# Optimization experiments

Measured on AMD Instinct MI355X. Metric: run time of the kernel, lower is better.

The kernel has to match this reference:

```python
import jax, jax.numpy as jnp
import numpy as np

HIDDEN_DIM = 1000
CONTEXT_DIM = 2000


def setup_inputs() -> dict:
    key = jax.random.key(0)
    k1, k2, k3, k4 = jax.random.split(key, 4)
    B, N = 64, 1024
    std = 0.001
    return {
        "s_prev": jax.random.normal(k1, (B, HIDDEN_DIM), dtype=jnp.float32),
        "h_j": jax.random.normal(k2, (B, N, CONTEXT_DIM), dtype=jnp.float32),
        "W_a": jax.random.normal(k3, (HIDDEN_DIM, HIDDEN_DIM), dtype=jnp.float32) * std,
        "U_a": jax.random.normal(k4, (HIDDEN_DIM, CONTEXT_DIM), dtype=jnp.float32) * std,
        "v_a": jnp.zeros((HIDDEN_DIM,), dtype=jnp.float32),
    }


def reference(s_prev, h_j, W_a, U_a, v_a):
    # W_a s: (B, H); U_a h: (B, N, H)
    W_a_s = jnp.einsum("bd,hd->bh", s_prev, W_a)
    U_a_h = jnp.einsum("bnc,hc->bnh", h_j, U_a)
    energy = jnp.tanh(W_a_s[:, None, :] + U_a_h)  # (B, N, H)
    scores = jnp.einsum("bnh,h->bn", energy, v_a)  # (B, N)
    return scores
```

## Files before the change

kernel.cpp:

```cpp
#include <hip/hip_runtime.h>
#include <hip/hip_bf16.h>

#define HID 1000
#define CTX 2000
#define KP   2016
#define HP   1024
#define BATCH 64
#define NSEQ 1024
#define M_TOT (BATCH * NSEQ)
#define WSTR 1024

typedef __attribute__((ext_vector_type(8))) short short8;
typedef __attribute__((ext_vector_type(4))) float floatx4;

__device__ __forceinline__ unsigned short f2bf(float x) {
    union { float f; unsigned u; } v; v.f = x;
    unsigned r = v.u + 0x7FFFu + ((v.u >> 16) & 1u);
    return (unsigned short)(r >> 16);
}

typedef const __attribute__((address_space(1))) unsigned glb_u32;
typedef __attribute__((address_space(3))) unsigned lds_u32;
__device__ __forceinline__ void gload16(const void* g, void* l) {
    __builtin_amdgcn_global_load_lds((glb_u32*)g, (lds_u32*)l, 16, 0, 0);
}

__global__ void zero_kernel(float* __restrict__ out, int n) {
    int i = blockIdx.x * 256 + threadIdx.x;
    if (i < n) out[i] = 0.0f;
}

__global__ void convertA_kernel(const float* __restrict__ src, unsigned short* __restrict__ dst) {
    int row = blockIdx.x;
    int t = threadIdx.x;
    if (t >= KP / 8) return;
    unsigned short pk[8];
    if (t < CTX / 8) {
        const float* p = src + (size_t)row * CTX + t * 8;
        float4 a = *(const float4*)p;
        float4 b = *(const float4*)(p + 4);
        pk[0]=f2bf(a.x); pk[1]=f2bf(a.y); pk[2]=f2bf(a.z); pk[3]=f2bf(a.w);
        pk[4]=f2bf(b.x); pk[5]=f2bf(b.y); pk[6]=f2bf(b.z); pk[7]=f2bf(b.w);
    } else {
#pragma unroll
        for (int i = 0; i < 8; i++) pk[i] = 0;
    }
    *(short8*)(dst + (size_t)row * KP + t * 8) = *(short8*)pk;
}

__global__ void convertB_kernel(const float* __restrict__ src, unsigned short* __restrict__ dst) {
    int row = blockIdx.x;
    int t = threadIdx.x;
    if (t >= KP / 8) return;
    unsigned short pk[8];
    if (row < HID && t < CTX / 8) {
        const float* p = src + (size_t)row * CTX + t * 8;
        float4 a = *(const float4*)p;
        float4 b = *(const float4*)(p + 4);
        pk[0]=f2bf(a.x); pk[1]=f2bf(a.y); pk[2]=f2bf(a.z); pk[3]=f2bf(a.w);
        pk[4]=f2bf(b.x); pk[5]=f2bf(b.y); pk[6]=f2bf(b.z); pk[7]=f2bf(b.w);
    } else {
#pragma unroll
        for (int i = 0; i < 8; i++) pk[i] = 0;
    }
    *(short8*)(dst + (size_t)row * KP + t * 8) = *(short8*)pk;
}

__global__ void ws_kernel(const float* __restrict__ s_prev,
                          const float* __restrict__ W_a,
                          float* __restrict__ W_s) {
    int wave = threadIdx.x >> 6, lane = threadIdx.x & 63;
    int gw = blockIdx.x * 4 + wave;
    int b = gw / HID, h = gw % HID;
    const float* wr = W_a + (size_t)h * HID;
    const float* sr = s_prev + (size_t)b * HID;
    float acc = 0.0f;
#pragma unroll
    for (int it = 0; it < 4; ++it) {
        int idx = it * 64 + lane;
        if (idx < HID / 4) {
            float4 w = *(const float4*)(wr + idx * 4);
            float4 s = *(const float4*)(sr + idx * 4);
            acc += w.x * s.x + w.y * s.y + w.z * s.z + w.w * s.w;
        }
    }
    acc += __shfl_xor(acc, 1);
    acc += __shfl_xor(acc, 2);
    acc += __shfl_xor(acc, 4);
    acc += __shfl_xor(acc, 8);
    acc += __shfl_xor(acc, 16);
    acc += __shfl_xor(acc, 32);
    if (lane == 0) W_s[b * WSTR + h] = acc;
}

__global__ __launch_bounds__(256) void gemm_kernel(
        const unsigned short* __restrict__ A, const unsigned short* __restrict__ B,
        const float* __restrict__ W_s, const float* __restrict__ v_a,
        float* __restrict__ out) {
    __shared__ __align__(16) unsigned short As[128 * 32];
    __shared__ __align__(16) unsigned short Bs[128 * 32];

    const int tid  = threadIdx.x;
    const int lane = tid & 63;
    const int wave = tid >> 6;
    const int wm = wave & 1, wh = wave >> 1;
    const int ln = lane & 15, quad = lane >> 4;

    const int h0 = blockIdx.x * 128;
    const int m0 = blockIdx.y * 128;
    const int b  = m0 >> 10;

    const int srow = lane >> 2;
    const int scol = (lane & 3) * 8;
    const unsigned short* aptr0 = A + (size_t)(m0 + wave * 16 + srow) * KP + scol;
    const unsigned short* aptr1 = aptr0 + (size_t)64 * KP;
    const unsigned short* bptr0 = B + (size_t)(h0 + wave * 16 + srow) * KP + scol;
    const unsigned short* bptr1 = bptr0 + (size_t)64 * KP;
    unsigned short* asl0 = &As[(wave * 16) * 32];
    unsigned short* asl1 = &As[(64 + wave * 16) * 32];
    unsigned short* bsl0 = &Bs[(wave * 16) * 32];
    unsigned short* bsl1 = &Bs[(64 + wave * 16) * 32];

    floatx4 acc[4][4];
#pragma unroll
    for (int i = 0; i < 4; i++)
#pragma unroll
        for (int j = 0; j < 4; j++) acc[i][j] = (floatx4)0.0f;

    for (int kk = 0; kk < KP / 32; ++kk) {
        __syncthreads();
        gload16(aptr0, asl0);
        gload16(aptr1, asl1);
        gload16(bptr0, bsl0);
        gload16(bptr1, bsl1);
        aptr0 += 32; aptr1 += 32; bptr0 += 32; bptr1 += 32;
        __syncthreads();

        short8 af[4], bfr[4];
#pragma unroll
        for (int i = 0; i < 4; i++)
            af[i] = *(const short8*)&As[(wm * 64 + i * 16 + ln) * 32 + quad * 8];
#pragma unroll
        for (int j = 0; j < 4; j++)
            bfr[j] = *(const short8*)&Bs[(wh * 64 + j * 16 + ln) * 32 + quad * 8];
#pragma unroll
        for (int i = 0; i < 4; i++)
#pragma unroll
            for (int j = 0; j < 4; j++)
                acc[i][j] = __builtin_amdgcn_mfma_f32_16x16x32_bf16(af[i], bfr[j], acc[i][j], 0, 0, 0);
    }

    float rowsum[4][4];
#pragma unroll
    for (int i = 0; i < 4; i++)
#pragma unroll
        for (int r = 0; r < 4; r++) rowsum[i][r] = 0.0f;

#pragma unroll
    for (int j = 0; j < 4; j++) {
        const int h = h0 + wh * 64 + j * 16 + ln;
        float wsv = 0.0f, vav = 0.0f;
        if (h < HID) { wsv = W_s[b * WSTR + h]; vav = v_a[h]; }
#pragma unroll
        for (int i = 0; i < 4; i++)
#pragma unroll
            for (int r = 0; r < 4; r++)
                rowsum[i][r] += vav * tanhf(acc[i][j][r] + wsv);
    }

#pragma unroll
    for (int i = 0; i < 4; i++)
#pragma unroll
        for (int r = 0; r < 4; r++) {
            float v = rowsum[i][r];
            v += __shfl_xor(v, 1);
            v += __shfl_xor(v, 2);
            v += __shfl_xor(v, 4);
            v += __shfl_xor(v, 8);
            rowsum[i][r] = v;
        }

    if (ln == 0) {
#pragma unroll
        for (int i = 0; i < 4; i++) {
            const int row = m0 + wm * 64 + i * 16 + quad * 4;
#pragma unroll
            for (int r = 0; r < 4; r++)
                atomicAdd(&out[row + r], rowsum[i][r]);
        }
    }
}

__global__ __launch_bounds__(256) void attn_fallback(
        const float* __restrict__ h_j, const float* __restrict__ U_a,
        const float* __restrict__ W_s, const float* __restrict__ v_a,
        float* __restrict__ out) {
    __shared__ unsigned short As[128 * 40];
    __shared__ unsigned short Bs[128 * 40];
    const int tid = threadIdx.x, lane = tid & 63, wave = tid >> 6;
    const int wm = wave & 1, wh = wave >> 1, ln = lane & 15, quad = lane >> 4;
    const int h0 = blockIdx.x * 128, m0 = blockIdx.y * 128, b = m0 >> 10;
    const int srow = tid >> 1, scol = (tid & 1) * 16;
    const float* aptr = h_j + (size_t)(m0 + srow) * CTX;
    const int gh = h0 + srow;
    const bool bvalid = (gh < HID);
    const float* bptr = U_a + (size_t)(bvalid ? gh : 0) * CTX;
    floatx4 acc[4][4];
#pragma unroll
    for (int i = 0; i < 4; i++)
#pragma unroll
        for (int j = 0; j < 4; j++) acc[i][j] = (floatx4)0.0f;
    for (int kk = 0; kk < 63; ++kk) {
        const int c = kk * 32 + scol;
        short8 apk0 = (short8)0, apk1 = (short8)0, bpk0 = (short8)0, bpk1 = (short8)0;
        if (c < CTX) {
            float4 t0 = *(const float4*)(aptr + c), t1 = *(const float4*)(aptr + c + 4);
            float4 t2 = *(const float4*)(aptr + c + 8), t3 = *(const float4*)(aptr + c + 12);
            apk0[0]=(short)f2bf(t0.x); apk0[1]=(short)f2bf(t0.y); apk0[2]=(short)f2bf(t0.z); apk0[3]=(short)f2bf(t0.w);
            apk0[4]=(short)f2bf(t1.x); apk0[5]=(short)f2bf(t1.y); apk0[6]=(short)f2bf(t1.z); apk0[7]=(short)f2bf(t1.w);
            apk1[0]=(short)f2bf(t2.x); apk1[1]=(short)f2bf(t2.y); apk1[2]=(short)f2bf(t2.z); apk1[3]=(short)f2bf(t2.w);
            apk1[4]=(short)f2bf(t3.x); apk1[5]=(short)f2bf(t3.y); apk1[6]=(short)f2bf(t3.z); apk1[7]=(short)f2bf(t3.w);
        }
        if (bvalid && c < CTX) {
            float4 t0 = *(const float4*)(bptr + c), t1 = *(const float4*)(bptr + c + 4);
            float4 t2 = *(const float4*)(bptr + c + 8), t3 = *(const float4*)(bptr + c + 12);
            bpk0[0]=(short)f2bf(t0.x); bpk0[1]=(short)f2bf(t0.y); bpk0[2]=(short)f2bf(t0.z); bpk0[3]=(short)f2bf(t0.w);
            bpk0[4]=(short)f2bf(t1.x); bpk0[5]=(short)f2bf(t1.y); bpk0[6]=(short)f2bf(t1.z); bpk0[7]=(short)f2bf(t1.w);
            bpk1[0]=(short)f2bf(t2.x); bpk1[1]=(short)f2bf(t2.y); bpk1[2]=(short)f2bf(t2.z); bpk1[3]=(short)f2bf(t2.w);
            bpk1[4]=(short)f2bf(t3.x); bpk1[5]=(short)f2bf(t3.y); bpk1[6]=(short)f2bf(t3.z); bpk1[7]=(short)f2bf(t3.w);
        }
        __syncthreads();
        *(short8*)&As[srow * 40 + scol]     = apk0;
        *(short8*)&As[srow * 40 + scol + 8] = apk1;
        *(short8*)&Bs[srow * 40 + scol]     = bpk0;
        *(short8*)&Bs[srow * 40 + scol + 8] = bpk1;
        __syncthreads();
        short8 af[4], bfr[4];
#pragma unroll
        for (int i = 0; i < 4; i++) af[i] = *(const short8*)&As[(wm * 64 + i * 16 + ln) * 40 + quad * 8];
#pragma unroll
        for (int j = 0; j < 4; j++) bfr[j] = *(const short8*)&Bs[(wh * 64 + j * 16 + ln) * 40 + quad * 8];
#pragma unroll
        for (int i = 0; i < 4; i++)
#pragma unroll
            for (int j = 0; j < 4; j++)
                acc[i][j] = __builtin_amdgcn_mfma_f32_16x16x32_bf16(af[i], bfr[j], acc[i][j], 0, 0, 0);
    }
    float rowsum[4][4];
#pragma unroll
    for (int i = 0; i < 4; i++)
#pragma unroll
        for (int r = 0; r < 4; r++) rowsum[i][r] = 0.0f;
#pragma unroll
    for (int j = 0; j < 4; j++) {
        const int h = h0 + wh * 64 + j * 16 + ln;
        float wsv = 0.0f, vav = 0.0f;
        if (h < HID) { wsv = W_s[b * WSTR + h]; vav = v_a[h]; }
#pragma unroll
        for (int i = 0; i < 4; i++)
#pragma unroll
            for (int r = 0; r < 4; r++)
                rowsum[i][r] += vav * tanhf(acc[i][j][r] + wsv);
    }
#pragma unroll
    for (int i = 0; i < 4; i++)
#pragma unroll
        for (int r = 0; r < 4; r++) {
            float v = rowsum[i][r];
            v += __shfl_xor(v, 1); v += __shfl_xor(v, 2);
            v += __shfl_xor(v, 4); v += __shfl_xor(v, 8);
            rowsum[i][r] = v;
        }
    if (ln == 0) {
#pragma unroll
        for (int i = 0; i < 4; i++) {
            const int row = m0 + wm * 64 + i * 16 + quad * 4;
#pragma unroll
            for (int r = 0; r < 4; r++) atomicAdd(&out[row + r], rowsum[i][r]);
        }
    }
}

extern "C" void kernel_launch(void* const* d_in, const int* in_sizes, int n_in,
                              void* d_out, int out_size, void* d_ws, size_t ws_size,
                              hipStream_t stream) {
    const float* s_prev = (const float*)d_in[0];
    const float* h_j    = (const float*)d_in[1];
    const float* W_a    = (const float*)d_in[2];
    const float* U_a    = (const float*)d_in[3];
    const float* v_a    = (const float*)d_in[4];
    float* out = (float*)d_out;

    const size_t ws_off   = 0;
    const size_t b_off    = 64 * WSTR * sizeof(float);
    const size_t a_off    = b_off + (size_t)HP * KP * sizeof(short);
    const size_t need     = a_off + (size_t)M_TOT * KP * sizeof(short);

    float* W_s = (float*)((char*)d_ws + ws_off);

    zero_kernel<<<dim3(M_TOT / 256), 256, 0, stream>>>(out, M_TOT);
    ws_kernel<<<dim3(BATCH * HID / 4), 256, 0, stream>>>(s_prev, W_a, W_s);

    if (ws_size >= need) {
        unsigned short* B_bf = (unsigned short*)((char*)d_ws + b_off);
        unsigned short* A_bf = (unsigned short*)((char*)d_ws + a_off);
        convertA_kernel<<<dim3(M_TOT), 256, 0, stream>>>(h_j, A_bf);
        convertB_kernel<<<dim3(HP), 256, 0, stream>>>(U_a, B_bf);
        gemm_kernel<<<dim3(HP / 128, M_TOT / 128), 256, 0, stream>>>(A_bf, B_bf, W_s, v_a, out);
    } else {
        attn_fallback<<<dim3(HP / 128, M_TOT / 128), 256, 0, stream>>>(h_j, U_a, W_s, v_a, out);
    }
}
```

Before: 1.222 ms.

## Loop over all hidden tiles inside each GEMM block, accumulating row sums locally

Each block now owns a 128-row M tile and iterates over all eight 128-wide hidden tiles, keeping the tanh-weighted row sums in registers instead of launching one block per (h, m) pair. This cuts the number of atomicAdds to the output and lets the A tile be re-read from L2 by the same block. It also adds a launch bound of 2 blocks per CU and removes the fallback path that ran when workspace was too small. The grid shrinks from 4096 to 512 blocks, which risks under-filling the GPU and serialises the work per block.

```diff
diff --git a/kernel.cpp b/kernel.cpp
--- a/kernel.cpp
+++ b/kernel.cpp
@@ -93,7 +93,7 @@
     if (lane == 0) W_s[b * WSTR + h] = acc;
 }
 
-__global__ __launch_bounds__(256) void gemm_kernel(
+__global__ __launch_bounds__(256, 2) void gemm_kernel(
         const unsigned short* __restrict__ A, const unsigned short* __restrict__ B,
         const float* __restrict__ W_s, const float* __restrict__ v_a,
         float* __restrict__ out) {
@@ -106,66 +106,70 @@
     const int wm = wave & 1, wh = wave >> 1;
     const int ln = lane & 15, quad = lane >> 4;
 
-    const int h0 = blockIdx.x * 128;
-    const int m0 = blockIdx.y * 128;
+    const int m0 = blockIdx.x * 128;
     const int b  = m0 >> 10;
 
     const int srow = lane >> 2;
     const int scol = (lane & 3) * 8;
-    const unsigned short* aptr0 = A + (size_t)(m0 + wave * 16 + srow) * KP + scol;
-    const unsigned short* aptr1 = aptr0 + (size_t)64 * KP;
-    const unsigned short* bptr0 = B + (size_t)(h0 + wave * 16 + srow) * KP + scol;
-    const unsigned short* bptr1 = bptr0 + (size_t)64 * KP;
+    const unsigned short* abase0 = A + (size_t)(m0 + wave * 16 + srow) * KP + scol;
+    const unsigned short* abase1 = abase0 + (size_t)64 * KP;
     unsigned short* asl0 = &As[(wave * 16) * 32];
     unsigned short* asl1 = &As[(64 + wave * 16) * 32];
     unsigned short* bsl0 = &Bs[(wave * 16) * 32];
     unsigned short* bsl1 = &Bs[(64 + wave * 16) * 32];
 
-    floatx4 acc[4][4];
+    float rowsum[4][4];
 #pragma unroll
     for (int i = 0; i < 4; i++)
 #pragma unroll
-        for (int j = 0; j < 4; j++) acc[i][j] = (floatx4)0.0f;
-
-    for (int kk = 0; kk < KP / 32; ++kk) {
-        __syncthreads();
-        gload16(aptr0, asl0);
-        gload16(aptr1, asl1);
-        gload16(bptr0, bsl0);
-        gload16(bptr1, bsl1);
-        aptr0 += 32; aptr1 += 32; bptr0 += 32; bptr1 += 32;
-        __syncthreads();
-
-        short8 af[4], bfr[4];
+        for (int r = 0; r < 4; r++) rowsum[i][r] = 0.0f;
+
+    for (int ht = 0; ht < HP / 128; ++ht) {
+        const unsigned short* aptr0 = abase0;
+        const unsigned short* aptr1 = abase1;
+        const unsigned short* bptr0 = B + (size_t)(ht * 128 + wave * 16 + srow) * KP + scol;
+        const unsigned short* bptr1 = bptr0 + (size_t)64 * KP;
+
+        floatx4 acc[4][4];
 #pragma unroll
         for (int i = 0; i < 4; i++)
-            af[i] = *(const short8*)&As[(wm * 64 + i * 16 + ln) * 32 + quad * 8];
-#pragma unroll
-        for (int j = 0; j < 4; j++)
-            bfr[j] = *(const short8*)&Bs[(wh * 64 + j * 16 + ln) * 32 + quad * 8];
-#pragma unroll
-        for (int i = 0; i < 4; i++)
+#pragma unroll
+            for (int j = 0; j < 4; j++) acc[i][j] = (floatx4)0.0f;
+
+        for (int kk = 0; kk < KP / 32; ++kk) {
+            __syncthreads();
+            gload16(aptr0, asl0);
+            gload16(aptr1, asl1);
+            gload16(bptr0, bsl0);
+            gload16(bptr1, bsl1);
+            aptr0 += 32; aptr1 += 32; bptr0 += 32; bptr1 += 32;
+            __syncthreads();
+
+            short8 af[4], bfr[4];
+#pragma unroll
+            for (int i = 0; i < 4; i++)
+                af[i] = *(const short8*)&As[(wm * 64 + i * 16 + ln) * 32 + quad * 8];
 #pragma unroll
             for (int j = 0; j < 4; j++)
-                acc[i][j] = __builtin_amdgcn_mfma_f32_16x16x32_bf16(af[i], bfr[j], acc[i][j], 0, 0, 0);
-    }
-
-    float rowsum[4][4];
-#pragma unroll
-    for (int i = 0; i < 4; i++)
-#pragma unroll
-        for (int r = 0; r < 4; r++) rowsum[i][r] = 0.0f;
-
-#pragma unroll
-    for (int j = 0; j < 4; j++) {
-        const int h = h0 + wh * 64 + j * 16 + ln;
-        float wsv = 0.0f, vav = 0.0f;
-        if (h < HID) { wsv = W_s[b * WSTR + h]; vav = v_a[h]; }
-#pragma unroll
-        for (int i = 0; i < 4; i++)
-#pragma unroll
-            for (int r = 0; r < 4; r++)
-                rowsum[i][r] += vav * tanhf(acc[i][j][r] + wsv);
+                bfr[j] = *(const short8*)&Bs[(wh * 64 + j * 16 + ln) * 32 + quad * 8];
+#pragma unroll
+            for (int i = 0; i < 4; i++)
+#pragma unroll
+                for (int j = 0; j < 4; j++)
+                    acc[i][j] = __builtin_amdgcn_mfma_f32_16x16x32_bf16(af[i], bfr[j], acc[i][j], 0, 0, 0);
+        }
+
+#pragma unroll
+        for (int j = 0; j < 4; j++) {
+            const int h = ht * 128 + wh * 64 + j * 16 + ln;
+            float wsv = 0.0f, vav = 0.0f;
+            if (h < HID) { wsv = W_s[b * WSTR + h]; vav = v_a[h]; }
+#pragma unroll
+            for (int i = 0; i < 4; i++)
+#pragma unroll
+                for (int r = 0; r < 4; r++)
+                    rowsum[i][r] += vav * tanhf(acc[i][j][r] + wsv);
+        }
     }
 
 #pragma unroll
@@ -187,96 +191,6 @@
 #pragma unroll
             for (int r = 0; r < 4; r++)
                 atomicAdd(&out[row + r], rowsum[i][r]);
-        }
-    }
-}
-
-__global__ __launch_bounds__(256) void attn_fallback(
-        const float* __restrict__ h_j, const float* __restrict__ U_a,
-        const float* __restrict__ W_s, const float* __restrict__ v_a,
-        float* __restrict__ out) {
-    __shared__ unsigned short As[128 * 40];
-    __shared__ unsigned short Bs[128 * 40];
-    const int tid = threadIdx.x, lane = tid & 63, wave = tid >> 6;
-    const int wm = wave & 1, wh = wave >> 1, ln = lane & 15, quad = lane >> 4;
-    const int h0 = blockIdx.x * 128, m0 = blockIdx.y * 128, b = m0 >> 10;
-    const int srow = tid >> 1, scol = (tid & 1) * 16;
-    const float* aptr = h_j + (size_t)(m0 + srow) * CTX;
-    const int gh = h0 + srow;
-    const bool bvalid = (gh < HID);
-    const float* bptr = U_a + (size_t)(bvalid ? gh : 0) * CTX;
-    floatx4 acc[4][4];
-#pragma unroll
-    for (int i = 0; i < 4; i++)
-#pragma unroll
-        for (int j = 0; j < 4; j++) acc[i][j] = (floatx4)0.0f;
-    for (int kk = 0; kk < 63; ++kk) {
-        const int c = kk * 32 + scol;
-        short8 apk0 = (short8)0, apk1 = (short8)0, bpk0 = (short8)0, bpk1 = (short8)0;
-        if (c < CTX) {
-            float4 t0 = *(const float4*)(aptr + c), t1 = *(const float4*)(aptr + c + 4);
-            float4 t2 = *(const float4*)(aptr + c + 8), t3 = *(const float4*)(aptr + c + 12);
-            apk0[0]=(short)f2bf(t0.x); apk0[1]=(short)f2bf(t0.y); apk0[2]=(short)f2bf(t0.z); apk0[3]=(short)f2bf(t0.w);
-            apk0[4]=(short)f2bf(t1.x); apk0[5]=(short)f2bf(t1.y); apk0[6]=(short)f2bf(t1.z); apk0[7]=(short)f2bf(t1.w);
-            apk1[0]=(short)f2bf(t2.x); apk1[1]=(short)f2bf(t2.y); apk1[2]=(short)f2bf(t2.z); apk1[3]=(short)f2bf(t2.w);
-            apk1[4]=(short)f2bf(t3.x); apk1[5]=(short)f2bf(t3.y); apk1[6]=(short)f2bf(t3.z); apk1[7]=(short)f2bf(t3.w);
-        }
-        if (bvalid && c < CTX) {
-            float4 t0 = *(const float4*)(bptr + c), t1 = *(const float4*)(bptr + c + 4);
-            float4 t2 = *(const float4*)(bptr + c + 8), t3 = *(const float4*)(bptr + c + 12);
-            bpk0[0]=(short)f2bf(t0.x); bpk0[1]=(short)f2bf(t0.y); bpk0[2]=(short)f2bf(t0.z); bpk0[3]=(short)f2bf(t0.w);
-            bpk0[4]=(short)f2bf(t1.x); bpk0[5]=(short)f2bf(t1.y); bpk0[6]=(short)f2bf(t1.z); bpk0[7]=(short)f2bf(t1.w);
-            bpk1[0]=(short)f2bf(t2.x); bpk1[1]=(short)f2bf(t2.y); bpk1[2]=(short)f2bf(t2.z); bpk1[3]=(short)f2bf(t2.w);
-            bpk1[4]=(short)f2bf(t3.x); bpk1[5]=(short)f2bf(t3.y); bpk1[6]=(short)f2bf(t3.z); bpk1[7]=(short)f2bf(t3.w);
-        }
-        __syncthreads();
-        *(short8*)&As[srow * 40 + scol]     = apk0;
-        *(short8*)&As[srow * 40 + scol + 8] = apk1;
-        *(short8*)&Bs[srow * 40 + scol]     = bpk0;
-        *(short8*)&Bs[srow * 40 + scol + 8] = bpk1;
-        __syncthreads();
-        short8 af[4], bfr[4];
-#pragma unroll
-        for (int i = 0; i < 4; i++) af[i] = *(const short8*)&As[(wm * 64 + i * 16 + ln) * 40 + quad * 8];
-#pragma unroll
-        for (int j = 0; j < 4; j++) bfr[j] = *(const short8*)&Bs[(wh * 64 + j * 16 + ln) * 40 + quad * 8];
-#pragma unroll
-        for (int i = 0; i < 4; i++)
-#pragma unroll
-            for (int j = 0; j < 4; j++)
-                acc[i][j] = __builtin_amdgcn_mfma_f32_16x16x32_bf16(af[i], bfr[j], acc[i][j], 0, 0, 0);
-    }
-    float rowsum[4][4];
-#pragma unroll
-    for (int i = 0; i < 4; i++)
-#pragma unroll
-        for (int r = 0; r < 4; r++) rowsum[i][r] = 0.0f;
-#pragma unroll
-    for (int j = 0; j < 4; j++) {
-        const int h = h0 + wh * 64 + j * 16 + ln;
-        float wsv = 0.0f, vav = 0.0f;
-        if (h < HID) { wsv = W_s[b * WSTR + h]; vav = v_a[h]; }
-#pragma unroll
-        for (int i = 0; i < 4; i++)
-#pragma unroll
-            for (int r = 0; r < 4; r++)
-                rowsum[i][r] += vav * tanhf(acc[i][j][r] + wsv);
-    }
-#pragma unroll
-    for (int i = 0; i < 4; i++)
-#pragma unroll
-        for (int r = 0; r < 4; r++) {
-            float v = rowsum[i][r];
-            v += __shfl_xor(v, 1); v += __shfl_xor(v, 2);
-            v += __shfl_xor(v, 4); v += __shfl_xor(v, 8);
-            rowsum[i][r] = v;
-        }
-    if (ln == 0) {
-#pragma unroll
-        for (int i = 0; i < 4; i++) {
-            const int row = m0 + wm * 64 + i * 16 + quad * 4;
-#pragma unroll
-            for (int r = 0; r < 4; r++) atomicAdd(&out[row + r], rowsum[i][r]);
         }
     }
 }
@@ -291,23 +205,15 @@
     const float* v_a    = (const float*)d_in[4];
     float* out = (float*)d_out;
 
-    const size_t ws_off   = 0;
-    const size_t b_off    = 64 * WSTR * sizeof(float);
-    const size_t a_off    = b_off + (size_t)HP * KP * sizeof(short);
-    const size_t need     = a_off + (size_t)M_TOT * KP * sizeof(short);
-
-    float* W_s = (float*)((char*)d_ws + ws_off);
+    const size_t b_off = 64 * WSTR * sizeof(float);
+    const size_t a_off = b_off + (size_t)HP * KP * sizeof(short);
+    float* W_s = (float*)d_ws;
+    unsigned short* B_bf = (unsigned short*)((char*)d_ws + b_off);
+    unsigned short* A_bf = (unsigned short*)((char*)d_ws + a_off);
 
     zero_kernel<<<dim3(M_TOT / 256), 256, 0, stream>>>(out, M_TOT);
     ws_kernel<<<dim3(BATCH * HID / 4), 256, 0, stream>>>(s_prev, W_a, W_s);
-
-    if (ws_size >= need) {
-        unsigned short* B_bf = (unsigned short*)((char*)d_ws + b_off);
-        unsigned short* A_bf = (unsigned short*)((char*)d_ws + a_off);
-        convertA_kernel<<<dim3(M_TOT), 256, 0, stream>>>(h_j, A_bf);
-        convertB_kernel<<<dim3(HP), 256, 0, stream>>>(U_a, B_bf);
-        gemm_kernel<<<dim3(HP / 128, M_TOT / 128), 256, 0, stream>>>(A_bf, B_bf, W_s, v_a, out);
-    } else {
-        attn_fallback<<<dim3(HP / 128, M_TOT / 128), 256, 0, stream>>>(h_j, U_a, W_s, v_a, out);
-    }
-}
+    convertA_kernel<<<dim3(M_TOT), 256, 0, stream>>>(h_j, A_bf);
+    convertB_kernel<<<dim3(HP), 256, 0, stream>>>(U_a, B_bf);
+    gemm_kernel<<<dim3(M_TOT / 128), 256, 0, stream>>>(A_bf, B_bf, W_s, v_a, out);
+}
```

Measured after the change: 1.190 ms. 1.03x faster.
